# Performance work log

Measured on AMD Instinct MI355X. Metric: run time of the kernel, lower is better.

Reference implementation:

```python
import jax, jax.numpy as jnp
import numpy as np
import math

STEP_SIZE = 1.0


def setup_inputs() -> dict:
    key = jax.random.key(0)
    ks = jax.random.split(key, 6)
    B, L, C, H, O = 4096, 256, 8, 128, 1
    n_int = L - 1
    coeffs = jax.random.normal(ks[0], (B, n_int, 4 * C), dtype=jnp.float32) * 0.1

    def lin(k, i, o):
        kw, kb = jax.random.split(k)
        s = 1.0 / math.sqrt(i)
        W = jax.random.uniform(kw, (i, o), minval=-s, maxval=s, dtype=jnp.float32)
        b = jax.random.uniform(kb, (o,), minval=-s, maxval=s, dtype=jnp.float32)
        return W, b

    W_init, b_init = lin(ks[1], C, H)
    W1, b1 = lin(ks[2], H, H)
    W2, b2 = lin(ks[3], H, H)
    W3, b3 = lin(ks[4], H, H * C)
    W_out, b_out = lin(ks[5], H, O)
    return dict(coeffs=coeffs, W_init=W_init, b_init=b_init, W1=W1, b1=b1,
                W2=W2, b2=b2, W3=W3, b3=b3, W_out=W_out, b_out=b_out)


def reference(coeffs, W_init, b_init, W1, b1, W2, b2, W3, b3, W_out, b_out):
    B, n_int, four_c = coeffs.shape
    C = four_c // 4
    H = W1.shape[0]
    # torchcde CubicSpline coefficient layout: a, b, two_c, three_d
    a, bcoef, two_c, three_d = jnp.split(coeffs, 4, axis=-1)  # each (B, n_int, C)
    knots = jnp.arange(n_int + 1, dtype=coeffs.dtype)  # t = linspace(0, n_int, n_int+1)
    T = float(n_int)

    def X_deriv(t):
        # torchcde _interpret_t: bucketize(t, knots)-1 clamped; here knots uniform
        idx = jnp.clip(jnp.searchsorted(knots, t, side='left') - 1, 0, n_int - 1)
        frac = t - knots[idx]
        return bcoef[:, idx] + (two_c[:, idx] + three_d[:, idx] * frac) * frac  # (B, C)

    def ode_f(t, z):
        # CDEFunc: Linear->Softplus x2, Linear->Tanh, reshape to (B, H, C)
        h = jax.nn.softplus(z @ W1 + b1)
        h = jax.nn.softplus(h @ W2 + b2)
        f = jnp.tanh(h @ W3 + b3).reshape(B, H, C)
        return jnp.einsum('bhc,bc->bh', f, X_deriv(t))  # f(z) @ dX/dt

    # torchdiffeq fixed-grid rk4 with step_size (3/8 rule: rk4_alt_step_func)
    n_steps = int(math.ceil(T / STEP_SIZE))
    ts = jnp.minimum(jnp.arange(n_steps + 1, dtype=coeffs.dtype) * STEP_SIZE, T)
    t0s, dts = ts[:-1], ts[1:] - ts[:-1]

    z0 = a[:, 0] @ W_init + b_init  # X.evaluate(interval[0]) == a at first knot

    def step(z, td):
        t0, dt = td
        k1 = ode_f(t0, z)
        k2 = ode_f(t0 + dt / 3, z + dt * k1 / 3)
        k3 = ode_f(t0 + dt * 2 / 3, z + dt * (k2 - k1 / 3))
        k4 = ode_f(t0 + dt, z + dt * (k1 - k2 + k3))
        return z + dt * (k1 + 3.0 * (k2 + k3) + k4) / 8.0, None

    zT, _ = jax.lax.scan(step, z0, (t0s, dts))
    return zT @ W_out + b_out
```

## Files before the change

kernel.cpp:

```cpp
#include <hip/hip_runtime.h>

#define NINT  255
#define BM    16
#define PITCH 136

typedef __bf16 bf16x8 __attribute__((ext_vector_type(8)));
typedef float  f32x4  __attribute__((ext_vector_type(4)));

#define MFMA(a, b, c) __builtin_amdgcn_mfma_f32_16x16x32_bf16((a), (b), (c), 0, 0, 0)

__device__ __forceinline__ unsigned short f2b(float f) {
    __bf16 b = (__bf16)f;
    return __builtin_bit_cast(unsigned short, b);
}

__device__ __forceinline__ float sp_f(float x) {
    float e = __builtin_amdgcn_exp2f(x * 1.4426950408889634f);
    float y = __builtin_amdgcn_logf(1.0f + e) * 0.6931471805599453f;
    return (x > 80.0f) ? x : y;
}

__device__ __forceinline__ float tanh_f(float x) {
    float e = __builtin_amdgcn_exp2f(x * 2.8853900817779268f);
    float r = __builtin_amdgcn_rcpf(e + 1.0f);
    return fmaf(-2.0f, r, 1.0f);
}

__global__ void prep_frags(const float* __restrict__ W1, const float* __restrict__ W2,
                           const float* __restrict__ W3,
                           unsigned short* __restrict__ W1f, unsigned short* __restrict__ W2f,
                           unsigned short* __restrict__ W3f) {
    const int e = blockIdx.x * 256 + threadIdx.x;
    const int i = e & 7;
    const int l = (e >> 3) & 63;
    const int t = (e >> 9) & 3;
    const int n = e >> 11;
    const int k = 32 * t + ((l >> 4) & 3) * 8 + i;
    const int c = l & 15;
    if (e < 16384) {
        W1f[e] = f2b(W1[k * 128 + 16 * n + c]);
        W2f[e] = f2b(W2[k * 128 + 16 * n + c]);
    }
    W3f[e] = f2b(W3[k * 1024 + 16 * n + c]);
}

__global__ __launch_bounds__(512, 2)
void cde_mfma(const float* __restrict__ coeffs,
              const float* __restrict__ W_init, const float* __restrict__ b_init,
              const float* __restrict__ b1, const float* __restrict__ b2,
              const float* __restrict__ b3,
              const float* __restrict__ W_out, const float* __restrict__ b_out,
              const unsigned short* __restrict__ w1f, const unsigned short* __restrict__ w2f,
              const unsigned short* __restrict__ w3f,
              float* __restrict__ out)
{
    __shared__ __align__(16) unsigned short W3r_lds[65536];
    __shared__ __align__(16) unsigned short Zs [BM * PITCH];
    __shared__ __align__(16) unsigned short H1s[BM * PITCH];
    __shared__ __align__(16) unsigned short H2s[BM * PITCH];
    __shared__ __align__(16) float Xds[2][4][16][8];
    __shared__ __align__(16) float b3s[1024];
    __shared__ __align__(16) float Outp[16][16];

    const int tid     = threadIdx.x;
    const int rowbase = blockIdx.x * BM;
    const int l       = tid & 63;
    const int w       = tid >> 6;
    const int batch   = l & 15;
    const int g       = (l >> 4) & 3;
    const int hb      = g >> 1;
    const int chB     = 4 * (g & 1);
    const int koff    = g * 8;

    for (int k4 = tid; k4 < 8192; k4 += 512)
        ((uint4*)W3r_lds)[k4] = ((const uint4*)(w3f + 32 * 2048))[k4];
    for (int k = tid; k < 1024; k += 512) b3s[k] = b3[k];

    const bf16x8* w1v = (const bf16x8*)w1f;
    const bf16x8* w2v = (const bf16x8*)w2f;
    const bf16x8* w3v = (const bf16x8*)w3f;
    bf16x8 w1r[4], w2r[4], w3g[4][4];
    #pragma unroll
    for (int t = 0; t < 4; ++t) {
        w1r[t] = w1v[(w * 4 + t) * 64 + l];
        w2r[t] = w2v[(w * 4 + t) * 64 + l];
    }
    #pragma unroll
    for (int jl = 0; jl < 4; ++jl)
        #pragma unroll
        for (int t = 0; t < 4; ++t)
            w3g[jl][t] = w3v[((8 * jl + w) * 4 + t) * 64 + l];

    const float b1r = b1[16 * w + batch];
    const float b2r = b2[16 * w + batch];

    float zb[8], k1r[8], k2r[8], k3r[8];
    {
        const float* ap = coeffs + (size_t)(rowbase + batch) * (NINT * 32);
        float av[8];
        #pragma unroll
        for (int c = 0; c < 8; ++c) av[c] = ap[c];
        #pragma unroll
        for (int jl = 0; jl < 8; ++jl) {
            const int h = 16 * jl + 2 * w + hb;
            float z = b_init[h];
            #pragma unroll
            for (int c = 0; c < 8; ++c) z = fmaf(av[c], W_init[c * 128 + h], z);
            zb[jl] = z;
            if ((g & 1) == 0) Zs[batch * PITCH + h] = f2b(z);
        }
    }
    __syncthreads();

    const bf16x8* w3rv = (const bf16x8*)W3r_lds;

    #pragma unroll 1
    for (int step = 0; step < NINT; ++step) {
        const int par = step & 1;
        if (tid < 128) {
            const int m = tid >> 3, c = tid & 7;
            const float* cp = coeffs + (size_t)(rowbase + m) * (NINT * 32);
            float s1;
            if (step == 0) s1 = cp[8 + c];
            else {
                const int i0 = (step - 1) * 32;
                s1 = cp[i0 + 8 + c] + cp[i0 + 16 + c] + cp[i0 + 24 + c];
            }
            const int ik = step * 32;
            const float bB = cp[ik + 8 + c];
            const float tc = cp[ik + 16 + c];
            const float td = cp[ik + 24 + c];
            Xds[par][0][m][c] = s1;
            Xds[par][1][m][c] = bB + (tc + td * (1.0f/3.0f)) * (1.0f/3.0f);
            Xds[par][2][m][c] = bB + (tc + td * (2.0f/3.0f)) * (2.0f/3.0f);
            Xds[par][3][m][c] = bB + tc + td;
        }

        #pragma unroll 1
        for (int st = 0; st < 4; ++st) {
            {
                bf16x8 a[4];
                #pragma unroll
                for (int t = 0; t < 4; ++t)
                    a[t] = *(const bf16x8*)(Zs + batch * PITCH + t * 32 + koff);
                f32x4 acc0 = {b1r, b1r, b1r, b1r};
                #pragma unroll
                for (int t = 0; t < 4; ++t) acc0 = MFMA(a[t], w1r[t], acc0);
                #pragma unroll
                for (int i = 0; i < 4; ++i)
                    H1s[(g * 4 + i) * PITCH + 16 * w + batch] = f2b(sp_f(acc0[i]));
            }
            __syncthreads();

            {
                bf16x8 a[4];
                #pragma unroll
                for (int t = 0; t < 4; ++t)
                    a[t] = *(const bf16x8*)(H1s + batch * PITCH + t * 32 + koff);
                f32x4 acc0 = {b2r, b2r, b2r, b2r};
                #pragma unroll
                for (int t = 0; t < 4; ++t) acc0 = MFMA(a[t], w2r[t], acc0);
                #pragma unroll
                for (int i = 0; i < 4; ++i)
                    H2s[(g * 4 + i) * PITCH + 16 * w + batch] = f2b(sp_f(acc0[i]));
            }
            __syncthreads();

            {
                bf16x8 bfr[4];
                #pragma unroll
                for (int t = 0; t < 4; ++t)
                    bfr[t] = *(const bf16x8*)(H2s + batch * PITCH + t * 32 + koff);

                f32x4 acc[8];
                #pragma unroll
                for (int jl = 0; jl < 8; ++jl)
                    acc[jl] = *(const f32x4*)&b3s[16 * (8 * jl + w) + 4 * g];

                #pragma unroll
                for (int jl = 0; jl < 4; ++jl)
                    #pragma unroll
                    for (int t = 0; t < 4; ++t)
                        acc[jl] = MFMA(w3g[jl][t], bfr[t], acc[jl]);

                #pragma unroll
                for (int jl = 4; jl < 8; ++jl)
                    #pragma unroll
                    for (int t = 0; t < 4; ++t)
                        acc[jl] = MFMA(w3rv[(((jl - 4) * 8 + w) * 4 + t) * 64 + l], bfr[t], acc[jl]);

                const f32x4 xdv = *(const f32x4*)&Xds[par][st][batch][chB];
                #pragma unroll
                for (int jl = 0; jl < 8; ++jl) {
                    float p = 0.0f;
                    #pragma unroll
                    for (int i = 0; i < 4; ++i)
                        p = fmaf(tanh_f(acc[jl][i]), xdv[i], p);
                    p += __shfl_xor(p, 16, 64);
                    float znew;
                    if (st == 0)      { k1r[jl] = p; znew = zb[jl] + p * (1.0f/3.0f); }
                    else if (st == 1) { k2r[jl] = p; znew = zb[jl] + p - k1r[jl] * (1.0f/3.0f); }
                    else if (st == 2) { k3r[jl] = p; znew = zb[jl] + k1r[jl] - k2r[jl] + p; }
                    else { zb[jl] = fmaf(k1r[jl] + 3.0f * (k2r[jl] + k3r[jl]) + p, 0.125f, zb[jl]); znew = zb[jl]; }
                    if ((g & 1) == 0)
                        Zs[batch * PITCH + 16 * jl + 2 * w + hb] = f2b(znew);
                }
            }
            __syncthreads();
        }
    }

    if ((g & 1) == 0) {
        float prt = 0.0f;
        #pragma unroll
        for (int jl = 0; jl < 8; ++jl)
            prt = fmaf(zb[jl], W_out[16 * jl + 2 * w + hb], prt);
        Outp[2 * w + hb][batch] = prt;
    }
    __syncthreads();
    if (tid < 16) {
        float s = b_out[0];
        #pragma unroll
        for (int p = 0; p < 16; ++p) s += Outp[p][tid];
        out[rowbase + tid] = s;
    }
}

extern "C" void kernel_launch(void* const* d_in, const int* in_sizes, int n_in,
                              void* d_out, int out_size, void* d_ws, size_t ws_size,
                              hipStream_t stream) {
    const float* coeffs = (const float*)d_in[0];
    const float* W_init = (const float*)d_in[1];
    const float* b_init = (const float*)d_in[2];
    const float* W1     = (const float*)d_in[3];
    const float* b1     = (const float*)d_in[4];
    const float* W2     = (const float*)d_in[5];
    const float* b2     = (const float*)d_in[6];
    const float* W3     = (const float*)d_in[7];
    const float* b3     = (const float*)d_in[8];
    const float* W_out  = (const float*)d_in[9];
    const float* b_out  = (const float*)d_in[10];
    float* outp = (float*)d_out;

    unsigned short* w1f = (unsigned short*)d_ws;
    unsigned short* w2f = w1f + 16384;
    unsigned short* w3f = w2f + 16384;

    hipLaunchKernelGGL(prep_frags, dim3(512), dim3(256), 0, stream, W1, W2, W3, w1f, w2f, w3f);
    hipLaunchKernelGGL(cde_mfma, dim3(4096 / BM), dim3(512), 0, stream,
                       coeffs, W_init, b_init, b1, b2, b3, W_out, b_out,
                       w1f, w2f, w3f, outp);
}
```

Measured before the change: 3.013 ms.

## Keep spline derivatives and b3 in registers, prefetch next interval, unroll RK stages

Each lane now loads the spline coefficients it needs straight from global memory into registers, prefetching the next interval one step ahead. The dX/dt values for each RK4 stage are computed in registers, which removes the 128-thread Xds LDS staging and its branch. The b3 bias moves from LDS into per-thread registers, and the four stages are fully unrolled through a macro so the stage-specific branches resolve at compile time. The cost is higher register pressure under launch_bounds(512,2), with a risk of spills, plus redundant global loads across lanes.

Measured after the change: 2.550 ms, median of 2. 1.18x faster.

```diff
diff --git a/kernel.cpp b/kernel.cpp
--- a/kernel.cpp
+++ b/kernel.cpp
@@ -44,6 +44,65 @@
     W3f[e] = f2b(W3[k * 1024 + 16 * n + c]);
 }
 
+#define STAGE_BODY(ST, XD)                                                       \
+{                                                                                \
+    bf16x8 a0[4];                                                                \
+    _Pragma("unroll")                                                            \
+    for (int t = 0; t < 4; ++t)                                                  \
+        a0[t] = *(const bf16x8*)(Zs + batch * PITCH + t * 32 + koff);            \
+    f32x4 h1 = {b1r, b1r, b1r, b1r};                                             \
+    _Pragma("unroll")                                                            \
+    for (int t = 0; t < 4; ++t) h1 = MFMA(a0[t], w1r[t], h1);                    \
+    _Pragma("unroll")                                                            \
+    for (int i = 0; i < 4; ++i)                                                  \
+        H1s[(g * 4 + i) * PITCH + 16 * w + batch] = f2b(sp_f(h1[i]));            \
+    __syncthreads();                                                             \
+    bf16x8 a1[4];                                                                \
+    _Pragma("unroll")                                                            \
+    for (int t = 0; t < 4; ++t)                                                  \
+        a1[t] = *(const bf16x8*)(H1s + batch * PITCH + t * 32 + koff);           \
+    f32x4 h2 = {b2r, b2r, b2r, b2r};                                             \
+    _Pragma("unroll")                                                            \
+    for (int t = 0; t < 4; ++t) h2 = MFMA(a1[t], w2r[t], h2);                    \
+    _Pragma("unroll")                                                            \
+    for (int i = 0; i < 4; ++i)                                                  \
+        H2s[(g * 4 + i) * PITCH + 16 * w + batch] = f2b(sp_f(h2[i]));            \
+    __syncthreads();                                                             \
+    bf16x8 bfr[4];                                                               \
+    _Pragma("unroll")                                                            \
+    for (int t = 0; t < 4; ++t)                                                  \
+        bfr[t] = *(const bf16x8*)(H2s + batch * PITCH + t * 32 + koff);          \
+    f32x4 acc[8];                                                                \
+    _Pragma("unroll")                                                            \
+    for (int jl = 0; jl < 4; ++jl) {                                             \
+        acc[jl] = MFMA(w3g[jl][0], bfr[0], b3r8[jl]);                            \
+        _Pragma("unroll")                                                        \
+        for (int t = 1; t < 4; ++t) acc[jl] = MFMA(w3g[jl][t], bfr[t], acc[jl]); \
+    }                                                                            \
+    _Pragma("unroll")                                                            \
+    for (int jl = 4; jl < 8; ++jl) {                                             \
+        acc[jl] = MFMA(w3rv[(((jl - 4) * 8 + w) * 4 + 0) * 64 + l], bfr[0], b3r8[jl]); \
+        _Pragma("unroll")                                                        \
+        for (int t = 1; t < 4; ++t)                                              \
+            acc[jl] = MFMA(w3rv[(((jl - 4) * 8 + w) * 4 + t) * 64 + l], bfr[t], acc[jl]); \
+    }                                                                            \
+    _Pragma("unroll")                                                            \
+    for (int jl = 0; jl < 8; ++jl) {                                             \
+        float p = 0.0f;                                                          \
+        _Pragma("unroll")                                                        \
+        for (int i = 0; i < 4; ++i) p = fmaf(tanh_f(acc[jl][i]), (XD)[i], p);    \
+        p += __shfl_xor(p, 16, 64);                                              \
+        float znew;                                                              \
+        if (ST == 0)      { k1r[jl] = p; znew = zb[jl] + p * (1.0f/3.0f); }      \
+        else if (ST == 1) { k2r[jl] = p; znew = zb[jl] + p - k1r[jl] * (1.0f/3.0f); } \
+        else if (ST == 2) { k3r[jl] = p; znew = zb[jl] + k1r[jl] - k2r[jl] + p; } \
+        else { zb[jl] = fmaf(k1r[jl] + 3.0f*(k2r[jl] + k3r[jl]) + p, 0.125f, zb[jl]); znew = zb[jl]; } \
+        if ((g & 1) == 0)                                                        \
+            Zs[batch * PITCH + 16 * jl + 2 * w + hb] = f2b(znew);                \
+    }                                                                            \
+    __syncthreads();                                                             \
+}
+
 __global__ __launch_bounds__(512, 2)
 void cde_mfma(const float* __restrict__ coeffs,
               const float* __restrict__ W_init, const float* __restrict__ b_init,
@@ -58,8 +117,6 @@
     __shared__ __align__(16) unsigned short Zs [BM * PITCH];
     __shared__ __align__(16) unsigned short H1s[BM * PITCH];
     __shared__ __align__(16) unsigned short H2s[BM * PITCH];
-    __shared__ __align__(16) float Xds[2][4][16][8];
-    __shared__ __align__(16) float b3s[1024];
     __shared__ __align__(16) float Outp[16][16];
 
     const int tid     = threadIdx.x;
@@ -74,7 +131,6 @@
 
     for (int k4 = tid; k4 < 8192; k4 += 512)
         ((uint4*)W3r_lds)[k4] = ((const uint4*)(w3f + 32 * 2048))[k4];
-    for (int k = tid; k < 1024; k += 512) b3s[k] = b3[k];
 
     const bf16x8* w1v = (const bf16x8*)w1f;
     const bf16x8* w2v = (const bf16x8*)w2f;
@@ -93,6 +149,10 @@
 
     const float b1r = b1[16 * w + batch];
     const float b2r = b2[16 * w + batch];
+    f32x4 b3r8[8];
+    #pragma unroll
+    for (int jl = 0; jl < 8; ++jl)
+        b3r8[jl] = *(const f32x4*)&b3[16 * (8 * jl + w) + 4 * g];
 
     float zb[8], k1r[8], k2r[8], k3r[8];
     {
@@ -110,104 +170,40 @@
             if ((g & 1) == 0) Zs[batch * PITCH + h] = f2b(z);
         }
     }
+
+    const float* cpx = coeffs + (size_t)(rowbase + batch) * (NINT * 32) + chB;
+    f32x4 bB  = *(const f32x4*)(cpx + 8);
+    f32x4 tcv = *(const f32x4*)(cpx + 16);
+    f32x4 tdv = *(const f32x4*)(cpx + 24);
+    f32x4 xd0 = bB;
+
+    const bf16x8* w3rv = (const bf16x8*)W3r_lds;
     __syncthreads();
-
-    const bf16x8* w3rv = (const bf16x8*)W3r_lds;
 
     #pragma unroll 1
     for (int step = 0; step < NINT; ++step) {
-        const int par = step & 1;
-        if (tid < 128) {
-            const int m = tid >> 3, c = tid & 7;
-            const float* cp = coeffs + (size_t)(rowbase + m) * (NINT * 32);
-            float s1;
-            if (step == 0) s1 = cp[8 + c];
-            else {
-                const int i0 = (step - 1) * 32;
-                s1 = cp[i0 + 8 + c] + cp[i0 + 16 + c] + cp[i0 + 24 + c];
-            }
-            const int ik = step * 32;
-            const float bB = cp[ik + 8 + c];
-            const float tc = cp[ik + 16 + c];
-            const float td = cp[ik + 24 + c];
-            Xds[par][0][m][c] = s1;
-            Xds[par][1][m][c] = bB + (tc + td * (1.0f/3.0f)) * (1.0f/3.0f);
-            Xds[par][2][m][c] = bB + (tc + td * (2.0f/3.0f)) * (2.0f/3.0f);
-            Xds[par][3][m][c] = bB + tc + td;
+        const int nxt = (step + 1 < NINT) ? step + 1 : NINT - 1;
+        const float* cn = cpx + nxt * 32;
+        const f32x4 nbB = *(const f32x4*)(cn + 8);
+        const f32x4 ntc = *(const f32x4*)(cn + 16);
+        const f32x4 ntd = *(const f32x4*)(cn + 24);
+
+        STAGE_BODY(0, xd0)
+
+        f32x4 xd1, xd2, xd3;
+        #pragma unroll
+        for (int i = 0; i < 4; ++i) {
+            xd1[i] = bB[i] + (tcv[i] + tdv[i] * (1.0f/3.0f)) * (1.0f/3.0f);
+            xd2[i] = bB[i] + (tcv[i] + tdv[i] * (2.0f/3.0f)) * (2.0f/3.0f);
+            xd3[i] = bB[i] + tcv[i] + tdv[i];
         }
 
-        #pragma unroll 1
-        for (int st = 0; st < 4; ++st) {
-            {
-                bf16x8 a[4];
-                #pragma unroll
-                for (int t = 0; t < 4; ++t)
-                    a[t] = *(const bf16x8*)(Zs + batch * PITCH + t * 32 + koff);
-                f32x4 acc0 = {b1r, b1r, b1r, b1r};
-                #pragma unroll
-                for (int t = 0; t < 4; ++t) acc0 = MFMA(a[t], w1r[t], acc0);
-                #pragma unroll
-                for (int i = 0; i < 4; ++i)
-                    H1s[(g * 4 + i) * PITCH + 16 * w + batch] = f2b(sp_f(acc0[i]));
-            }
-            __syncthreads();
-
-            {
-                bf16x8 a[4];
-                #pragma unroll
-                for (int t = 0; t < 4; ++t)
-                    a[t] = *(const bf16x8*)(H1s + batch * PITCH + t * 32 + koff);
-                f32x4 acc0 = {b2r, b2r, b2r, b2r};
-                #pragma unroll
-                for (int t = 0; t < 4; ++t) acc0 = MFMA(a[t], w2r[t], acc0);
-                #pragma unroll
-                for (int i = 0; i < 4; ++i)
-                    H2s[(g * 4 + i) * PITCH + 16 * w + batch] = f2b(sp_f(acc0[i]));
-            }
-            __syncthreads();
-
-            {
-                bf16x8 bfr[4];
-                #pragma unroll
-                for (int t = 0; t < 4; ++t)
-                    bfr[t] = *(const bf16x8*)(H2s + batch * PITCH + t * 32 + koff);
-
-                f32x4 acc[8];
-                #pragma unroll
-                for (int jl = 0; jl < 8; ++jl)
-                    acc[jl] = *(const f32x4*)&b3s[16 * (8 * jl + w) + 4 * g];
-
-                #pragma unroll
-                for (int jl = 0; jl < 4; ++jl)
-                    #pragma unroll
-                    for (int t = 0; t < 4; ++t)
-                        acc[jl] = MFMA(w3g[jl][t], bfr[t], acc[jl]);
-
-                #pragma unroll
-                for (int jl = 4; jl < 8; ++jl)
-                    #pragma unroll
-                    for (int t = 0; t < 4; ++t)
-                        acc[jl] = MFMA(w3rv[(((jl - 4) * 8 + w) * 4 + t) * 64 + l], bfr[t], acc[jl]);
-
-                const f32x4 xdv = *(const f32x4*)&Xds[par][st][batch][chB];
-                #pragma unroll
-                for (int jl = 0; jl < 8; ++jl) {
-                    float p = 0.0f;
-                    #pragma unroll
-                    for (int i = 0; i < 4; ++i)
-                        p = fmaf(tanh_f(acc[jl][i]), xdv[i], p);
-                    p += __shfl_xor(p, 16, 64);
-                    float znew;
-                    if (st == 0)      { k1r[jl] = p; znew = zb[jl] + p * (1.0f/3.0f); }
-                    else if (st == 1) { k2r[jl] = p; znew = zb[jl] + p - k1r[jl] * (1.0f/3.0f); }
-                    else if (st == 2) { k3r[jl] = p; znew = zb[jl] + k1r[jl] - k2r[jl] + p; }
-                    else { zb[jl] = fmaf(k1r[jl] + 3.0f * (k2r[jl] + k3r[jl]) + p, 0.125f, zb[jl]); znew = zb[jl]; }
-                    if ((g & 1) == 0)
-                        Zs[batch * PITCH + 16 * jl + 2 * w + hb] = f2b(znew);
-                }
-            }
-            __syncthreads();
-        }
+        STAGE_BODY(1, xd1)
+        STAGE_BODY(2, xd2)
+        STAGE_BODY(3, xd3)
+
+        xd0 = xd3;
+        bB = nbB; tcv = ntc; tdv = ntd;
     }
 
     if ((g & 1) == 0) {
```
